# Performance work log

Measured on AMD Instinct MI355X. Metric: run time of the kernel, lower is better.

Reference implementation:

```python
import jax, jax.numpy as jnp
import numpy as np

B, H, S, DH = 2, 16, 2048, 64
MASK_FILL = -10000.0


def setup_inputs() -> dict:
    key = jax.random.key(0)
    kq, kk, kv = jax.random.split(key, 3)
    q = jax.random.normal(kq, (B, H, S, DH), dtype=jnp.float32)
    k = jax.random.normal(kk, (B, H, S, DH), dtype=jnp.float32)
    v = jax.random.normal(kv, (B, H, S, DH), dtype=jnp.float32)
    # causal mask: True where attention is disallowed (upper triangle)
    mask = jnp.triu(jnp.ones((S, S), dtype=jnp.bool_), k=1)
    return {"q": q, "k": k, "v": v, "mask": mask}


def reference(q, k, v, mask):
    scale = 1.0 / jnp.sqrt(jnp.asarray(k.shape[-1], dtype=q.dtype))
    # scores: [B, H, S_q, S_k]
    scores = jnp.einsum("bhqd,bhkd->bhqk", q, k) * scale
    # additive mask: masked_fill on a zeros [S_k, S_v] matrix -> -10000 where mask
    attn_bias = jnp.where(mask, jnp.asarray(MASK_FILL, dtype=k.dtype),
                          jnp.asarray(0.0, dtype=k.dtype))
    scores = scores + attn_bias  # broadcast over batch/heads
    attn = jax.nn.softmax(scores, axis=-1)
    # dropout_rate = 0.0 -> identity
    return jnp.einsum("bhqk,bhkd->bhqd", attn, v)
```

## Files before the change

### kernel.cpp

```cpp
#include <hip/hip_runtime.h>


#define S_LEN  2048
#define DHDIM  64
#define NHEADS 32
#define LDP    72
#define M2     23.083120654223414f
#define QSCALE 0.18033688011117658f
#define NSLOT  52

typedef __attribute__((ext_vector_type(8))) short bf16x8;
typedef __attribute__((ext_vector_type(4))) float f32x4;

#define RT(qt,k0,k1,sl) ((unsigned)(qt)<<24 | (unsigned)(k0)<<16 | (unsigned)(k1)<<8 | (unsigned)(sl))
__device__ __constant__ unsigned RTAB[63] = {
    RT(31,0,11,49),  RT(31,11,22,50), RT(30,0,11,46),  RT(21,0,11,20),
    RT(21,11,22,21), RT(20,0,11,18),  RT(10,0,11,255),
    RT(31,22,32,51), RT(30,11,21,47), RT(30,21,31,48), RT(29,0,10,43),
    RT(29,10,20,44), RT(29,20,30,45), RT(28,0,10,40),  RT(28,10,20,41),
    RT(27,0,10,37),  RT(20,11,21,19), RT(19,0,10,16),  RT(19,10,20,17),
    RT(18,0,10,14),  RT(9,0,10,255),
    RT(28,20,29,42), RT(27,10,19,38), RT(27,19,28,39), RT(26,0,9,34),
    RT(26,9,18,35),  RT(26,18,27,36), RT(25,0,9,31),   RT(25,9,18,32),
    RT(24,0,9,28),   RT(18,10,19,15), RT(17,0,9,12),   RT(17,9,18,13),
    RT(16,0,9,10),   RT(8,0,9,255),
    RT(25,18,26,33), RT(24,9,17,29),  RT(24,17,25,30), RT(23,0,8,25),
    RT(23,8,16,26),  RT(23,16,24,27), RT(22,0,8,22),   RT(22,8,16,23),
    RT(16,9,17,11),  RT(15,0,8,8),    RT(15,8,16,9),   RT(14,0,8,6),
    RT(7,0,8,255),
    RT(22,16,23,24), RT(14,8,15,7),   RT(13,0,7,4),    RT(13,7,14,5),
    RT(12,0,7,2),    RT(6,0,7,255),
    RT(12,7,13,3),   RT(11,0,6,0),    RT(11,6,12,1),   RT(5,0,6,255),
    RT(4,0,5,255),   RT(3,0,4,255),   RT(2,0,3,255),   RT(1,0,2,255),
    RT(0,0,1,255)};

__device__ __forceinline__ float fast_exp2(float x) {
#if __has_builtin(__builtin_amdgcn_exp2f)
    return __builtin_amdgcn_exp2f(x);
#else
    return exp2f(x);
#endif
}
__device__ __forceinline__ unsigned short f2bf(float f) {
    unsigned u = __float_as_uint(f);
    return (unsigned short)((u + 0x7fffu + ((u >> 16) & 1u)) >> 16);
}
__device__ __forceinline__ void ld8(const float* p, float* f) {
    float4 a = *(const float4*)p, b = *(const float4*)(p + 4);
    f[0]=a.x; f[1]=a.y; f[2]=a.z; f[3]=a.w; f[4]=b.x; f[5]=b.y; f[6]=b.z; f[7]=b.w;
}
__device__ __forceinline__ uint4 pack8(const float* f, float scale) {
    union { uint4 v; unsigned short s[8]; } w;
    #pragma unroll
    for (int j = 0; j < 8; j++) w.s[j] = f2bf(f[j] * scale);
    return w.v;
}
__device__ __forceinline__ unsigned packhi(float a, float b) {
#if __has_builtin(__builtin_amdgcn_perm)
    return __builtin_amdgcn_perm(__float_as_uint(b), __float_as_uint(a), 0x07060302u);
#else
    return (__float_as_uint(a) >> 16) | (__float_as_uint(b) & 0xffff0000u);
#endif
}

__global__ __launch_bounds__(256) void prep(
    const float* __restrict__ Qf, const float* __restrict__ Kf,
    const float* __restrict__ Vf, unsigned short* __restrict__ qb,
    unsigned short* __restrict__ kb, unsigned short* __restrict__ vtb)
{
    const int st = blockIdx.x, bh = blockIdx.y;
    __shared__ unsigned lt32[64][LDP / 2];
    const float* vp = Vf + ((size_t)bh * S_LEN + st * 64) * DHDIM;
    {
        const int c = threadIdx.x;
        const int sp = c >> 3;
        const int d0 = (c & 7) * 8;
        float fa[8], fb[8];
        ld8(vp + (2 * sp) * DHDIM + d0, fa);
        ld8(vp + (2 * sp + 1) * DHDIM + d0, fb);
        #pragma unroll
        for (int j = 0; j < 8; j++) {
            int d = d0 + j;
            int colw = (sp & 3) | ((((sp >> 2) ^ (d >> 3)) & 7) << 2);
            lt32[d][colw] = (unsigned)f2bf(fa[j]) | ((unsigned)f2bf(fb[j]) << 16);
        }
    }
    size_t off = ((size_t)(bh * 32 + st) * 4096) + (size_t)threadIdx.x * 16;
    float f[8];
    ld8(Qf + off, f);     *(uint4*)(qb + off)     = pack8(f, QSCALE);
    ld8(Qf + off + 8, f); *(uint4*)(qb + off + 8) = pack8(f, QSCALE);
    ld8(Kf + off, f);     *(uint4*)(kb + off)     = pack8(f, 1.0f);
    ld8(Kf + off + 8, f); *(uint4*)(kb + off + 8) = pack8(f, 1.0f);
    __syncthreads();
    unsigned short* op = vtb + (size_t)bh * DHDIM * S_LEN + st * 64;
    for (int c = threadIdx.x; c < 512; c += 256) {
        int d = c >> 3, q = c & 7;
        int colw = ((q ^ (d >> 3)) & 7) << 2;
        *(uint4*)(op + (size_t)d * S_LEN + q * 8) = *(const uint4*)&lt32[d][colw];
    }
}

__global__ __launch_bounds__(256) void fattn_splitk(
    const unsigned short* __restrict__ Qp, const unsigned short* __restrict__ Kp,
    const unsigned short* __restrict__ Vp,
    float* __restrict__ pO, float* __restrict__ pL, float* __restrict__ O)
{
    __shared__ unsigned short smem[192 * LDP];
    unsigned short (*ks)[LDP]  = (unsigned short(*)[LDP])smem;
    unsigned short (*vts)[LDP] = (unsigned short(*)[LDP])(smem + 64 * LDP);
    unsigned short (*qs)[LDP]  = (unsigned short(*)[LDP])(smem + 128 * LDP);
    unsigned short (*pst)[LDP] = qs;

    const int bh   = blockIdx.x;
    const unsigned e = RTAB[blockIdx.y];
    const int qt   = e >> 24;
    const int k0   = (e >> 16) & 255;
    const int k1   = (e >> 8) & 255;
    const int sl   = e & 255;
    const bool whole = (sl == 255);

    const int tid = threadIdx.x;
    const int wave = tid >> 6, lane = tid & 63;
    const int quad = lane >> 4, l16 = lane & 15;

    {
        const unsigned short* src = Qp + ((size_t)bh * S_LEN + qt * 64) * DHDIM;
        for (int c = tid; c < 512; c += 256) {
            int row = c >> 3, c8 = (c & 7) * 8;
            *(uint4*)&qs[row][c8] = *(const uint4*)(src + row * DHDIM + c8);
        }
    }
    __syncthreads();

    const int prow = wave * 16 + l16;
    const bf16x8 bq0 = *(const bf16x8*)&qs[prow][quad * 8];
    const bf16x8 bq1 = *(const bf16x8*)&qs[prow][32 + quad * 8];

    bf16x8 ones;
    #pragma unroll
    for (int j = 0; j < 8; j++) ones[j] = (short)0x3F80;

    f32x4 of[4];
    f32x4 of_l = (f32x4){0.f, 0.f, 0.f, 0.f};
    #pragma unroll
    for (int n = 0; n < 4; n++) of[n] = (f32x4){0.f, 0.f, 0.f, 0.f};

    const unsigned short* Kbh = Kp + (size_t)bh * S_LEN * DHDIM;
    const unsigned short* Vbh = Vp + (size_t)bh * DHDIM * S_LEN;
    const int sr = tid >> 3, sc = (tid & 7) * 8;
    uint4 kr0, kr1, vr0, vr1;
    {
        const unsigned short* ksrc = Kbh + (size_t)k0 * 64 * DHDIM;
        const unsigned short* vsrc = Vbh + k0 * 64;
        kr0 = *(const uint4*)(ksrc + sr * DHDIM + sc);
        kr1 = *(const uint4*)(ksrc + (sr + 32) * DHDIM + sc);
        vr0 = *(const uint4*)(vsrc + (size_t)sr * S_LEN + sc);
        vr1 = *(const uint4*)(vsrc + (size_t)(sr + 32) * S_LEN + sc);
    }

    for (int kt = k0; kt < k1; kt++) {
        __syncthreads();

        *(uint4*)&ks[sr][sc]       = kr0;
        *(uint4*)&ks[sr + 32][sc]  = kr1;
        *(uint4*)&vts[sr][sc]      = vr0;
        *(uint4*)&vts[sr + 32][sc] = vr1;

        if (kt + 1 < k1) {
            const unsigned short* ksrc = Kbh + (size_t)(kt + 1) * 64 * DHDIM;
            const unsigned short* vsrc = Vbh + (kt + 1) * 64;
            kr0 = *(const uint4*)(ksrc + sr * DHDIM + sc);
            kr1 = *(const uint4*)(ksrc + (sr + 32) * DHDIM + sc);
            vr0 = *(const uint4*)(vsrc + (size_t)sr * S_LEN + sc);
            vr1 = *(const uint4*)(vsrc + (size_t)(sr + 32) * S_LEN + sc);
        }
        __syncthreads();

        __builtin_amdgcn_s_setprio(1);
        f32x4 sf[4];
        #pragma unroll
        for (int n = 0; n < 4; n++) {
            bf16x8 ak0 = *(const bf16x8*)&ks[n * 16 + l16][quad * 8];
            bf16x8 ak1 = *(const bf16x8*)&ks[n * 16 + l16][32 + quad * 8];
            sf[n] = (f32x4){-M2, -M2, -M2, -M2};
            sf[n] = __builtin_amdgcn_mfma_f32_16x16x32_bf16(ak0, bq0, sf[n], 0, 0, 0);
            sf[n] = __builtin_amdgcn_mfma_f32_16x16x32_bf16(ak1, bq1, sf[n], 0, 0, 0);
        }
        __builtin_amdgcn_s_setprio(0);

        const bool diag = (kt == qt);
        #pragma unroll
        for (int n = 0; n < 4; n++) {
            float p[4];
            #pragma unroll
            for (int r = 0; r < 4; r++) {
                p[r] = fast_exp2(sf[n][r]);
                if (diag && (n * 16 + quad * 4 + r > prow)) p[r] = 0.f;
            }
            uint2 dw;
            dw.x = packhi(p[0], p[1]);
            dw.y = packhi(p[2], p[3]);
            *(uint2*)&pst[prow][n * 16 + quad * 4] = dw;
        }
        asm volatile("s_waitcnt lgkmcnt(0)" ::: "memory");

        __builtin_amdgcn_s_setprio(1);
        bf16x8 bp0 = *(const bf16x8*)&pst[prow][quad * 8];
        bf16x8 bp1 = *(const bf16x8*)&pst[prow][32 + quad * 8];
        of_l = __builtin_amdgcn_mfma_f32_16x16x32_bf16(ones, bp0, of_l, 0, 0, 0);
        of_l = __builtin_amdgcn_mfma_f32_16x16x32_bf16(ones, bp1, of_l, 0, 0, 0);
        #pragma unroll
        for (int n = 0; n < 4; n++) {
            bf16x8 av0 = *(const bf16x8*)&vts[n * 16 + l16][quad * 8];
            bf16x8 av1 = *(const bf16x8*)&vts[n * 16 + l16][32 + quad * 8];
            of[n] = __builtin_amdgcn_mfma_f32_16x16x32_bf16(av0, bp0, of[n], 0, 0, 0);
            of[n] = __builtin_amdgcn_mfma_f32_16x16x32_bf16(av1, bp1, of[n], 0, 0, 0);
        }
        __builtin_amdgcn_s_setprio(0);
    }

    if (whole) {
        const float inv = 1.f / of_l[0];
        float* op = O + ((size_t)bh * S_LEN + qt * 64 + prow) * DHDIM;
        #pragma unroll
        for (int n = 0; n < 4; n++)
            *(float4*)(op + n * 16 + quad * 4) = make_float4(
                of[n][0] * inv, of[n][1] * inv, of[n][2] * inv, of[n][3] * inv);
    } else {
        const int slot = bh * NSLOT + sl;
        if (quad == 0) pL[slot * 64 + prow] = of_l[0];
        float* op = pO + (size_t)slot * 4096 + prow * 64;
        #pragma unroll
        for (int n = 0; n < 4; n++)
            *(float4*)(op + n * 16 + quad * 4) =
                make_float4(of[n][0], of[n][1], of[n][2], of[n][3]);
    }
}

__global__ __launch_bounds__(256) void combine(
    const float* __restrict__ pO, const float* __restrict__ pL,
    float* __restrict__ O)
{
    const int qt = 11 + blockIdx.x, bh = blockIdx.y;
    int base, cnt;
    if (qt < 22) { base = (qt - 11) * 2;      cnt = 2; }
    else         { base = 22 + 3 * (qt - 22); cnt = 3; }
    const int sb = bh * NSLOT + base;
    const float* A = pO + (size_t)sb * 4096;
    float* out = O + ((size_t)bh * S_LEN + qt * 64) * DHDIM;
    #pragma unroll
    for (int k = 0; k < 4; k++) {
        int c = threadIdx.x + k * 256;
        int row = c >> 4;
        float l = pL[sb * 64 + row] + pL[(sb + 1) * 64 + row];
        float4 a = *(const float4*)(A + c * 4);
        float4 b = *(const float4*)(A + 4096 + c * 4);
        float4 s = make_float4(a.x + b.x, a.y + b.y, a.z + b.z, a.w + b.w);
        if (cnt == 3) {
            l += pL[(sb + 2) * 64 + row];
            float4 d = *(const float4*)(A + 8192 + c * 4);
            s = make_float4(s.x + d.x, s.y + d.y, s.z + d.z, s.w + d.w);
        }
        float inv = 1.f / l;
        *(float4*)(out + c * 4) = make_float4(
            s.x * inv, s.y * inv, s.z * inv, s.w * inv);
    }
}

template <bool PRE>
__global__ __launch_bounds__(256) void fattn_kernel(
    const void* __restrict__ Qp, const void* __restrict__ Kp,
    const void* __restrict__ Vp, float* __restrict__ O)
{
    __shared__ unsigned short smem[192 * LDP];
    unsigned short (*ks)[LDP]  = (unsigned short(*)[LDP])smem;
    unsigned short (*vts)[LDP] = (unsigned short(*)[LDP])(smem + 64 * LDP);
    unsigned short (*qs)[LDP]  = (unsigned short(*)[LDP])(smem + 128 * LDP);
    unsigned short (*pst)[LDP] = qs;

    const int id = blockIdx.y * 32 + blockIdx.x;
    const int g  = id >> 8;
    const int r8 = id & 255;
    const int bh = r8 >> 3;
    const int s8 = r8 & 7;
    const int qt = (g == 0) ? 31 - 2 * s8 : (g == 1) ? 2 * s8
                 : (g == 2) ? 30 - 2 * s8 : 2 * s8 + 1;

    const int tid = threadIdx.x;
    const int wave = tid >> 6, lane = tid & 63;
    const int quad = lane >> 4, l16 = lane & 15;

    if constexpr (PRE) {
        const unsigned short* src = (const unsigned short*)Qp
            + ((size_t)bh * S_LEN + qt * 64) * DHDIM;
        for (int c = tid; c < 512; c += 256) {
            int row = c >> 3, c8 = (c & 7) * 8;
            *(uint4*)&qs[row][c8] = *(const uint4*)(src + row * DHDIM + c8);
        }
    } else {
        const float* src = (const float*)Qp + ((size_t)bh * S_LEN + qt * 64) * DHDIM;
        for (int c = tid; c < 512; c += 256) {
            int row = c >> 3, c8 = (c & 7) * 8;
            float f[8]; ld8(src + row * DHDIM + c8, f);
            *(uint4*)&qs[row][c8] = pack8(f, QSCALE);
        }
    }
    __syncthreads();

    const int prow = wave * 16 + l16;
    const bf16x8 bq0 = *(const bf16x8*)&qs[prow][quad * 8];
    const bf16x8 bq1 = *(const bf16x8*)&qs[prow][32 + quad * 8];

    float l_p = 0.f;
    f32x4 of[4];
    #pragma unroll
    for (int n = 0; n < 4; n++) of[n] = (f32x4){0.f, 0.f, 0.f, 0.f};

    for (int kt = 0; kt <= qt; kt++) {
        __syncthreads();
        if constexpr (PRE) {
            const unsigned short* ksrc = (const unsigned short*)Kp
                + ((size_t)bh * S_LEN + kt * 64) * DHDIM;
            const unsigned short* vsrc = (const unsigned short*)Vp
                + (size_t)bh * DHDIM * S_LEN + kt * 64;
            for (int c = tid; c < 512; c += 256) {
                int row = c >> 3, c8 = (c & 7) * 8;
                *(uint4*)&ks[row][c8]  = *(const uint4*)(ksrc + row * DHDIM + c8);
                *(uint4*)&vts[row][c8] = *(const uint4*)(vsrc + (size_t)row * S_LEN + c8);
            }
        } else {
            const float* ksrc = (const float*)Kp + ((size_t)bh * S_LEN + kt * 64) * DHDIM;
            const float* vsrc = (const float*)Vp + ((size_t)bh * S_LEN + kt * 64) * DHDIM;
            for (int c = tid; c < 512; c += 256) {
                int row = c >> 3, c8 = (c & 7) * 8;
                float f[8];
                ld8(ksrc + row * DHDIM + c8, f);
                *(uint4*)&ks[row][c8] = pack8(f, 1.0f);
                ld8(vsrc + row * DHDIM + c8, f);
                #pragma unroll
                for (int j = 0; j < 8; j++) vts[c8 + j][row] = f2bf(f[j]);
            }
        }
        __syncthreads();

        f32x4 sf[4];
        #pragma unroll
        for (int n = 0; n < 4; n++) {
            bf16x8 ak0 = *(const bf16x8*)&ks[n * 16 + l16][quad * 8];
            bf16x8 ak1 = *(const bf16x8*)&ks[n * 16 + l16][32 + quad * 8];
            sf[n] = (f32x4){-M2, -M2, -M2, -M2};
            sf[n] = __builtin_amdgcn_mfma_f32_16x16x32_bf16(ak0, bq0, sf[n], 0, 0, 0);
            sf[n] = __builtin_amdgcn_mfma_f32_16x16x32_bf16(ak1, bq1, sf[n], 0, 0, 0);
        }

        const bool diag = (kt == qt);
        #pragma unroll
        for (int n = 0; n < 4; n++) {
            float p[4];
            #pragma unroll
            for (int r = 0; r < 4; r++) {
                p[r] = fast_exp2(sf[n][r]);
                if (diag && (n * 16 + quad * 4 + r > prow)) p[r] = 0.f;
                l_p += p[r];
            }
            uint2 dw;
            dw.x = packhi(p[0], p[1]);
            dw.y = packhi(p[2], p[3]);
            *(uint2*)&pst[prow][n * 16 + quad * 4] = dw;
        }
        asm volatile("s_waitcnt lgkmcnt(0)" ::: "memory");

        bf16x8 bp0 = *(const bf16x8*)&pst[prow][quad * 8];
        bf16x8 bp1 = *(const bf16x8*)&pst[prow][32 + quad * 8];
        #pragma unroll
        for (int n = 0; n < 4; n++) {
            bf16x8 av0 = *(const bf16x8*)&vts[n * 16 + l16][quad * 8];
            bf16x8 av1 = *(const bf16x8*)&vts[n * 16 + l16][32 + quad * 8];
            of[n] = __builtin_amdgcn_mfma_f32_16x16x32_bf16(av0, bp0, of[n], 0, 0, 0);
            of[n] = __builtin_amdgcn_mfma_f32_16x16x32_bf16(av1, bp1, of[n], 0, 0, 0);
        }
    }

    l_p += __shfl_xor(l_p, 16);
    l_p += __shfl_xor(l_p, 32);
    const float inv = 1.f / l_p;
    float* op = O + ((size_t)bh * S_LEN + qt * 64 + prow) * DHDIM;
    #pragma unroll
    for (int n = 0; n < 4; n++)
        *(float4*)(op + n * 16 + quad * 4) = make_float4(
            of[n][0] * inv, of[n][1] * inv, of[n][2] * inv, of[n][3] * inv);
}

extern "C" void kernel_launch(void* const* d_in, const int* in_sizes, int n_in,
                              void* d_out, int out_size, void* d_ws, size_t ws_size,
                              hipStream_t stream) {
    const float* Q = (const float*)d_in[0];
    const float* K = (const float*)d_in[1];
    const float* V = (const float*)d_in[2];
    float* O = (float*)d_out;
    const size_t N = (size_t)NHEADS * S_LEN * DHDIM;
    const size_t prepB  = 3 * N * sizeof(unsigned short);
    const size_t partB  = (size_t)NSLOT * 32 * (4096 + 64) * sizeof(float);

    if (d_ws && ws_size >= prepB + partB) {
        unsigned short* qb  = (unsigned short*)d_ws;
        unsigned short* kb  = qb + N;
        unsigned short* vtb = kb + N;
        float* pO = (float*)((char*)d_ws + prepB);
        float* pL = pO + (size_t)NSLOT * 32 * 4096;
        prep<<<dim3(S_LEN / 64, NHEADS), 256, 0, stream>>>(Q, K, V, qb, kb, vtb);
        fattn_splitk<<<dim3(32, 63), 256, 0, stream>>>(qb, kb, vtb, pO, pL, O);
        combine<<<dim3(21, 32), 256, 0, stream>>>(pO, pL, O);
    } else if (d_ws && ws_size >= prepB) {
        unsigned short* qb  = (unsigned short*)d_ws;
        unsigned short* kb  = qb + N;
        unsigned short* vtb = kb + N;
        prep<<<dim3(S_LEN / 64, NHEADS), 256, 0, stream>>>(Q, K, V, qb, kb, vtb);
        fattn_kernel<true><<<dim3(32, 32), 256, 0, stream>>>(qb, kb, vtb, O);
    } else {
        fattn_kernel<false><<<dim3(32, 32), 256, 0, stream>>>(Q, K, V, O);
    }
}
```

Measured before the change: 141.0 us.

## Process two K/V tiles per loop iteration with doubled shared buffers

The split-K attention loop now stages two 64-row K/V tiles per iteration into separate shared-memory buffers and prefetches the next two tiles into registers. This halves the number of barrier pairs per block and lets both QK^T MFMA batches issue back to back before the softmax/PV phases. In exchange, shared memory grows from 192 to 320 rows, and the extra prefetch registers and score accumulators raise register pressure, which may reduce occupancy.

Measured after the change: 144.7 us. 1.03x slower.

```diff
diff --git a/kernel.cpp b/kernel.cpp
--- a/kernel.cpp
+++ b/kernel.cpp
@@ -105,11 +105,13 @@
     const unsigned short* __restrict__ Vp,
     float* __restrict__ pO, float* __restrict__ pL, float* __restrict__ O)
 {
-    __shared__ unsigned short smem[192 * LDP];
-    unsigned short (*ks)[LDP]  = (unsigned short(*)[LDP])smem;
-    unsigned short (*vts)[LDP] = (unsigned short(*)[LDP])(smem + 64 * LDP);
-    unsigned short (*qs)[LDP]  = (unsigned short(*)[LDP])(smem + 128 * LDP);
-    unsigned short (*pst)[LDP] = qs;
+    __shared__ unsigned short smem[320 * LDP];
+    unsigned short (*ksA)[LDP]  = (unsigned short(*)[LDP])smem;
+    unsigned short (*ksB)[LDP]  = (unsigned short(*)[LDP])(smem + 64 * LDP);
+    unsigned short (*vtsA)[LDP] = (unsigned short(*)[LDP])(smem + 128 * LDP);
+    unsigned short (*vtsB)[LDP] = (unsigned short(*)[LDP])(smem + 192 * LDP);
+    unsigned short (*qs)[LDP]   = (unsigned short(*)[LDP])(smem + 256 * LDP);
+    unsigned short (*pst)[LDP]  = qs;
 
     const int bh   = blockIdx.x;
     const unsigned e = RTAB[blockIdx.y];
@@ -148,75 +150,142 @@
     const unsigned short* Kbh = Kp + (size_t)bh * S_LEN * DHDIM;
     const unsigned short* Vbh = Vp + (size_t)bh * DHDIM * S_LEN;
     const int sr = tid >> 3, sc = (tid & 7) * 8;
-    uint4 kr0, kr1, vr0, vr1;
+    uint4 krA0, krA1, vrA0, vrA1, krB0, krB1, vrB0, vrB1;
     {
         const unsigned short* ksrc = Kbh + (size_t)k0 * 64 * DHDIM;
         const unsigned short* vsrc = Vbh + k0 * 64;
-        kr0 = *(const uint4*)(ksrc + sr * DHDIM + sc);
-        kr1 = *(const uint4*)(ksrc + (sr + 32) * DHDIM + sc);
-        vr0 = *(const uint4*)(vsrc + (size_t)sr * S_LEN + sc);
-        vr1 = *(const uint4*)(vsrc + (size_t)(sr + 32) * S_LEN + sc);
-    }
-
-    for (int kt = k0; kt < k1; kt++) {
+        krA0 = *(const uint4*)(ksrc + sr * DHDIM + sc);
+        krA1 = *(const uint4*)(ksrc + (sr + 32) * DHDIM + sc);
+        vrA0 = *(const uint4*)(vsrc + (size_t)sr * S_LEN + sc);
+        vrA1 = *(const uint4*)(vsrc + (size_t)(sr + 32) * S_LEN + sc);
+    }
+    if (k0 + 1 < k1) {
+        const unsigned short* ksrc = Kbh + (size_t)(k0 + 1) * 64 * DHDIM;
+        const unsigned short* vsrc = Vbh + (k0 + 1) * 64;
+        krB0 = *(const uint4*)(ksrc + sr * DHDIM + sc);
+        krB1 = *(const uint4*)(ksrc + (sr + 32) * DHDIM + sc);
+        vrB0 = *(const uint4*)(vsrc + (size_t)sr * S_LEN + sc);
+        vrB1 = *(const uint4*)(vsrc + (size_t)(sr + 32) * S_LEN + sc);
+    }
+
+    for (int kt = k0; kt < k1; kt += 2) {
+        const bool hasB = (kt + 1 < k1);
         __syncthreads();
 
-        *(uint4*)&ks[sr][sc]       = kr0;
-        *(uint4*)&ks[sr + 32][sc]  = kr1;
-        *(uint4*)&vts[sr][sc]      = vr0;
-        *(uint4*)&vts[sr + 32][sc] = vr1;
-
-        if (kt + 1 < k1) {
-            const unsigned short* ksrc = Kbh + (size_t)(kt + 1) * 64 * DHDIM;
-            const unsigned short* vsrc = Vbh + (kt + 1) * 64;
-            kr0 = *(const uint4*)(ksrc + sr * DHDIM + sc);
-            kr1 = *(const uint4*)(ksrc + (sr + 32) * DHDIM + sc);
-            vr0 = *(const uint4*)(vsrc + (size_t)sr * S_LEN + sc);
-            vr1 = *(const uint4*)(vsrc + (size_t)(sr + 32) * S_LEN + sc);
+        *(uint4*)&ksA[sr][sc]       = krA0;
+        *(uint4*)&ksA[sr + 32][sc]  = krA1;
+        *(uint4*)&vtsA[sr][sc]      = vrA0;
+        *(uint4*)&vtsA[sr + 32][sc] = vrA1;
+        if (hasB) {
+            *(uint4*)&ksB[sr][sc]       = krB0;
+            *(uint4*)&ksB[sr + 32][sc]  = krB1;
+            *(uint4*)&vtsB[sr][sc]      = vrB0;
+            *(uint4*)&vtsB[sr + 32][sc] = vrB1;
+        }
+
+        if (kt + 2 < k1) {
+            const unsigned short* ksrc = Kbh + (size_t)(kt + 2) * 64 * DHDIM;
+            const unsigned short* vsrc = Vbh + (kt + 2) * 64;
+            krA0 = *(const uint4*)(ksrc + sr * DHDIM + sc);
+            krA1 = *(const uint4*)(ksrc + (sr + 32) * DHDIM + sc);
+            vrA0 = *(const uint4*)(vsrc + (size_t)sr * S_LEN + sc);
+            vrA1 = *(const uint4*)(vsrc + (size_t)(sr + 32) * S_LEN + sc);
+        }
+        if (kt + 3 < k1) {
+            const unsigned short* ksrc = Kbh + (size_t)(kt + 3) * 64 * DHDIM;
+            const unsigned short* vsrc = Vbh + (kt + 3) * 64;
+            krB0 = *(const uint4*)(ksrc + sr * DHDIM + sc);
+            krB1 = *(const uint4*)(ksrc + (sr + 32) * DHDIM + sc);
+            vrB0 = *(const uint4*)(vsrc + (size_t)sr * S_LEN + sc);
+            vrB1 = *(const uint4*)(vsrc + (size_t)(sr + 32) * S_LEN + sc);
         }
         __syncthreads();
 
         __builtin_amdgcn_s_setprio(1);
-        f32x4 sf[4];
+        f32x4 sfA[4], sfB[4];
         #pragma unroll
         for (int n = 0; n < 4; n++) {
-            bf16x8 ak0 = *(const bf16x8*)&ks[n * 16 + l16][quad * 8];
-            bf16x8 ak1 = *(const bf16x8*)&ks[n * 16 + l16][32 + quad * 8];
-            sf[n] = (f32x4){-M2, -M2, -M2, -M2};
-            sf[n] = __builtin_amdgcn_mfma_f32_16x16x32_bf16(ak0, bq0, sf[n], 0, 0, 0);
-            sf[n] = __builtin_amdgcn_mfma_f32_16x16x32_bf16(ak1, bq1, sf[n], 0, 0, 0);
+            bf16x8 ak0 = *(const bf16x8*)&ksA[n * 16 + l16][quad * 8];
+            bf16x8 ak1 = *(const bf16x8*)&ksA[n * 16 + l16][32 + quad * 8];
+            sfA[n] = (f32x4){-M2, -M2, -M2, -M2};
+            sfA[n] = __builtin_amdgcn_mfma_f32_16x16x32_bf16(ak0, bq0, sfA[n], 0, 0, 0);
+            sfA[n] = __builtin_amdgcn_mfma_f32_16x16x32_bf16(ak1, bq1, sfA[n], 0, 0, 0);
+        }
+        if (hasB) {
+            #pragma unroll
+            for (int n = 0; n < 4; n++) {
+                bf16x8 bk0 = *(const bf16x8*)&ksB[n * 16 + l16][quad * 8];
+                bf16x8 bk1 = *(const bf16x8*)&ksB[n * 16 + l16][32 + quad * 8];
+                sfB[n] = (f32x4){-M2, -M2, -M2, -M2};
+                sfB[n] = __builtin_amdgcn_mfma_f32_16x16x32_bf16(bk0, bq0, sfB[n], 0, 0, 0);
+                sfB[n] = __builtin_amdgcn_mfma_f32_16x16x32_bf16(bk1, bq1, sfB[n], 0, 0, 0);
+            }
         }
         __builtin_amdgcn_s_setprio(0);
 
-        const bool diag = (kt == qt);
-        #pragma unroll
-        for (int n = 0; n < 4; n++) {
-            float p[4];
-            #pragma unroll
-            for (int r = 0; r < 4; r++) {
-                p[r] = fast_exp2(sf[n][r]);
-                if (diag && (n * 16 + quad * 4 + r > prow)) p[r] = 0.f;
-            }
-            uint2 dw;
-            dw.x = packhi(p[0], p[1]);
-            dw.y = packhi(p[2], p[3]);
-            *(uint2*)&pst[prow][n * 16 + quad * 4] = dw;
-        }
-        asm volatile("s_waitcnt lgkmcnt(0)" ::: "memory");
-
-        __builtin_amdgcn_s_setprio(1);
-        bf16x8 bp0 = *(const bf16x8*)&pst[prow][quad * 8];
-        bf16x8 bp1 = *(const bf16x8*)&pst[prow][32 + quad * 8];
-        of_l = __builtin_amdgcn_mfma_f32_16x16x32_bf16(ones, bp0, of_l, 0, 0, 0);
-        of_l = __builtin_amdgcn_mfma_f32_16x16x32_bf16(ones, bp1, of_l, 0, 0, 0);
-        #pragma unroll
-        for (int n = 0; n < 4; n++) {
-            bf16x8 av0 = *(const bf16x8*)&vts[n * 16 + l16][quad * 8];
-            bf16x8 av1 = *(const bf16x8*)&vts[n * 16 + l16][32 + quad * 8];
-            of[n] = __builtin_amdgcn_mfma_f32_16x16x32_bf16(av0, bp0, of[n], 0, 0, 0);
-            of[n] = __builtin_amdgcn_mfma_f32_16x16x32_bf16(av1, bp1, of[n], 0, 0, 0);
-        }
-        __builtin_amdgcn_s_setprio(0);
+        {
+            const bool diag = (kt == qt);
+            #pragma unroll
+            for (int n = 0; n < 4; n++) {
+                float p[4];
+                #pragma unroll
+                for (int r = 0; r < 4; r++) {
+                    p[r] = fast_exp2(sfA[n][r]);
+                    if (diag && (n * 16 + quad * 4 + r > prow)) p[r] = 0.f;
+                }
+                uint2 dw;
+                dw.x = packhi(p[0], p[1]);
+                dw.y = packhi(p[2], p[3]);
+                *(uint2*)&pst[prow][n * 16 + quad * 4] = dw;
+            }
+            asm volatile("s_waitcnt lgkmcnt(0)" ::: "memory");
+
+            __builtin_amdgcn_s_setprio(1);
+            bf16x8 bp0 = *(const bf16x8*)&pst[prow][quad * 8];
+            bf16x8 bp1 = *(const bf16x8*)&pst[prow][32 + quad * 8];
+            of_l = __builtin_amdgcn_mfma_f32_16x16x32_bf16(ones, bp0, of_l, 0, 0, 0);
+            of_l = __builtin_amdgcn_mfma_f32_16x16x32_bf16(ones, bp1, of_l, 0, 0, 0);
+            #pragma unroll
+            for (int n = 0; n < 4; n++) {
+                bf16x8 av0 = *(const bf16x8*)&vtsA[n * 16 + l16][quad * 8];
+                bf16x8 av1 = *(const bf16x8*)&vtsA[n * 16 + l16][32 + quad * 8];
+                of[n] = __builtin_amdgcn_mfma_f32_16x16x32_bf16(av0, bp0, of[n], 0, 0, 0);
+                of[n] = __builtin_amdgcn_mfma_f32_16x16x32_bf16(av1, bp1, of[n], 0, 0, 0);
+            }
+            __builtin_amdgcn_s_setprio(0);
+        }
+
+        if (hasB) {
+            const bool diag = (kt + 1 == qt);
+            #pragma unroll
+            for (int n = 0; n < 4; n++) {
+                float p[4];
+                #pragma unroll
+                for (int r = 0; r < 4; r++) {
+                    p[r] = fast_exp2(sfB[n][r]);
+                    if (diag && (n * 16 + quad * 4 + r > prow)) p[r] = 0.f;
+                }
+                uint2 dw;
+                dw.x = packhi(p[0], p[1]);
+                dw.y = packhi(p[2], p[3]);
+                *(uint2*)&pst[prow][n * 16 + quad * 4] = dw;
+            }
+            asm volatile("s_waitcnt lgkmcnt(0)" ::: "memory");
+
+            __builtin_amdgcn_s_setprio(1);
+            bf16x8 bp0 = *(const bf16x8*)&pst[prow][quad * 8];
+            bf16x8 bp1 = *(const bf16x8*)&pst[prow][32 + quad * 8];
+            of_l = __builtin_amdgcn_mfma_f32_16x16x32_bf16(ones, bp0, of_l, 0, 0, 0);
+            of_l = __builtin_amdgcn_mfma_f32_16x16x32_bf16(ones, bp1, of_l, 0, 0, 0);
+            #pragma unroll
+            for (int n = 0; n < 4; n++) {
+                bf16x8 av0 = *(const bf16x8*)&vtsB[n * 16 + l16][quad * 8];
+                bf16x8 av1 = *(const bf16x8*)&vtsB[n * 16 + l16][32 + quad * 8];
+                of[n] = __builtin_amdgcn_mfma_f32_16x16x32_bf16(av0, bp0, of[n], 0, 0, 0);
+                of[n] = __builtin_amdgcn_mfma_f32_16x16x32_bf16(av1, bp1, of[n], 0, 0, 0);
+            }
+            __builtin_amdgcn_s_setprio(0);
+        }
     }
 
     if (whole) {
```

## Switch attention kernel to 32x32 MFMA tiles with software-pipelined PV stage

Applied to the files above, without the earlier changes.

Replaces the 16x16x32 MFMA tiling with 32x32x16 MFMAs. Each wave now covers a 32-query by 32-key quadrant, and Q fragments are loaded straight from global memory into registers instead of staging through LDS. The P·V product for the previous key tile is deferred one iteration, with double-buffered V and P LDS regions, so it overlaps with the next QK^T and exp stage and the explicit lgkmcnt wait goes away. The cost is more LDS per block, a launch-bounds occupancy hint, and an extra epilogue step to drain the last tile.

Measured after the change: 141.7 us. Within noise of the previous version (+0.5%).

```diff
diff --git a/kernel.cpp b/kernel.cpp
--- a/kernel.cpp
+++ b/kernel.cpp
@@ -11,6 +11,7 @@
 
 typedef __attribute__((ext_vector_type(8))) short bf16x8;
 typedef __attribute__((ext_vector_type(4))) float f32x4;
+typedef __attribute__((ext_vector_type(16))) float f32x16;
 
 #define RT(qt,k0,k1,sl) ((unsigned)(qt)<<24 | (unsigned)(k0)<<16 | (unsigned)(k1)<<8 | (unsigned)(sl))
 __device__ __constant__ unsigned RTAB[63] = {
@@ -100,16 +101,17 @@
     }
 }
 
-__global__ __launch_bounds__(256) void fattn_splitk(
+__global__ __launch_bounds__(256, 3) void fattn_splitk(
     const unsigned short* __restrict__ Qp, const unsigned short* __restrict__ Kp,
     const unsigned short* __restrict__ Vp,
     float* __restrict__ pO, float* __restrict__ pL, float* __restrict__ O)
 {
-    __shared__ unsigned short smem[192 * LDP];
-    unsigned short (*ks)[LDP]  = (unsigned short(*)[LDP])smem;
-    unsigned short (*vts)[LDP] = (unsigned short(*)[LDP])(smem + 64 * LDP);
-    unsigned short (*qs)[LDP]  = (unsigned short(*)[LDP])(smem + 128 * LDP);
-    unsigned short (*pst)[LDP] = qs;
+    __shared__ unsigned short smem[320 * LDP];
+    unsigned short (*ks)[LDP]   = (unsigned short(*)[LDP])smem;
+    unsigned short (*vtsA)[LDP] = (unsigned short(*)[LDP])(smem + 64 * LDP);
+    unsigned short (*vtsB)[LDP] = (unsigned short(*)[LDP])(smem + 128 * LDP);
+    unsigned short (*pstA)[LDP] = (unsigned short(*)[LDP])(smem + 192 * LDP);
+    unsigned short (*pstB)[LDP] = (unsigned short(*)[LDP])(smem + 256 * LDP);
 
     const int bh   = blockIdx.x;
     const unsigned e = RTAB[blockIdx.y];
@@ -119,31 +121,26 @@
     const int sl   = e & 255;
     const bool whole = (sl == 255);
 
-    const int tid = threadIdx.x;
+    const int tid  = threadIdx.x;
     const int wave = tid >> 6, lane = tid & 63;
-    const int quad = lane >> 4, l16 = lane & 15;
-
-    {
-        const unsigned short* src = Qp + ((size_t)bh * S_LEN + qt * 64) * DHDIM;
-        for (int c = tid; c < 512; c += 256) {
-            int row = c >> 3, c8 = (c & 7) * 8;
-            *(uint4*)&qs[row][c8] = *(const uint4*)(src + row * DHDIM + c8);
-        }
-    }
-    __syncthreads();
-
-    const int prow = wave * 16 + l16;
-    const bf16x8 bq0 = *(const bf16x8*)&qs[prow][quad * 8];
-    const bf16x8 bq1 = *(const bf16x8*)&qs[prow][32 + quad * 8];
+    const int q31  = lane & 31, hi = lane >> 5;
+    const int qh   = wave & 1, kh = wave >> 1;
+    const int qrow = qh * 32 + q31;
+
+    const unsigned short* qsrc = Qp + ((size_t)bh * S_LEN + qt * 64 + qrow) * DHDIM;
+    const bf16x8 bq0 = *(const bf16x8*)(qsrc + hi * 8);
+    const bf16x8 bq1 = *(const bf16x8*)(qsrc + 16 + hi * 8);
+    const bf16x8 bq2 = *(const bf16x8*)(qsrc + 32 + hi * 8);
+    const bf16x8 bq3 = *(const bf16x8*)(qsrc + 48 + hi * 8);
 
     bf16x8 ones;
     #pragma unroll
     for (int j = 0; j < 8; j++) ones[j] = (short)0x3F80;
 
-    f32x4 of[4];
-    f32x4 of_l = (f32x4){0.f, 0.f, 0.f, 0.f};
-    #pragma unroll
-    for (int n = 0; n < 4; n++) of[n] = (f32x4){0.f, 0.f, 0.f, 0.f};
+    f32x16 of, ofl;
+    #pragma unroll
+    for (int i = 0; i < 16; i++) { of[i] = 0.f; ofl[i] = 0.f; }
+    unsigned pdw[8];
 
     const unsigned short* Kbh = Kp + (size_t)bh * S_LEN * DHDIM;
     const unsigned short* Vbh = Vp + (size_t)bh * DHDIM * S_LEN;
@@ -161,11 +158,21 @@
     for (int kt = k0; kt < k1; kt++) {
         __syncthreads();
 
-        *(uint4*)&ks[sr][sc]       = kr0;
-        *(uint4*)&ks[sr + 32][sc]  = kr1;
-        *(uint4*)&vts[sr][sc]      = vr0;
-        *(uint4*)&vts[sr + 32][sc] = vr1;
-
+        *(uint4*)&ks[sr][sc]      = kr0;
+        *(uint4*)&ks[sr + 32][sc] = kr1;
+        {
+            unsigned short (*vts)[LDP] = (kt & 1) ? vtsB : vtsA;
+            *(uint4*)&vts[sr][sc]      = vr0;
+            *(uint4*)&vts[sr + 32][sc] = vr1;
+        }
+        if (kt > k0) {
+            unsigned short (*pst)[LDP] = ((kt - 1) & 1) ? pstB : pstA;
+            const int cb = kh * 32 + 4 * hi;
+            *(uint2*)&pst[qrow][cb +  0] = *(uint2*)&pdw[0];
+            *(uint2*)&pst[qrow][cb +  8] = *(uint2*)&pdw[2];
+            *(uint2*)&pst[qrow][cb + 16] = *(uint2*)&pdw[4];
+            *(uint2*)&pst[qrow][cb + 24] = *(uint2*)&pdw[6];
+        }
         if (kt + 1 < k1) {
             const unsigned short* ksrc = Kbh + (size_t)(kt + 1) * 64 * DHDIM;
             const unsigned short* vsrc = Vbh + (kt + 1) * 64;
@@ -176,64 +183,93 @@
         }
         __syncthreads();
 
+        if (kt > k0) {
+            const unsigned short (*pst)[LDP] = ((kt - 1) & 1) ? pstB : pstA;
+            const unsigned short (*vts)[LDP] = ((kt - 1) & 1) ? vtsB : vtsA;
+            __builtin_amdgcn_s_setprio(1);
+            #pragma unroll
+            for (int s = 0; s < 4; s++) {
+                bf16x8 av = *(const bf16x8*)&vts[kh * 32 + q31][s * 16 + hi * 8];
+                bf16x8 bp = *(const bf16x8*)&pst[qrow][s * 16 + hi * 8];
+                of  = __builtin_amdgcn_mfma_f32_32x32x16_bf16(av, bp, of, 0, 0, 0);
+                ofl = __builtin_amdgcn_mfma_f32_32x32x16_bf16(ones, bp, ofl, 0, 0, 0);
+            }
+            __builtin_amdgcn_s_setprio(0);
+        }
+
+        f32x16 sf;
+        #pragma unroll
+        for (int i = 0; i < 16; i++) sf[i] = -M2;
         __builtin_amdgcn_s_setprio(1);
-        f32x4 sf[4];
-        #pragma unroll
-        for (int n = 0; n < 4; n++) {
-            bf16x8 ak0 = *(const bf16x8*)&ks[n * 16 + l16][quad * 8];
-            bf16x8 ak1 = *(const bf16x8*)&ks[n * 16 + l16][32 + quad * 8];
-            sf[n] = (f32x4){-M2, -M2, -M2, -M2};
-            sf[n] = __builtin_amdgcn_mfma_f32_16x16x32_bf16(ak0, bq0, sf[n], 0, 0, 0);
-            sf[n] = __builtin_amdgcn_mfma_f32_16x16x32_bf16(ak1, bq1, sf[n], 0, 0, 0);
+        {
+            bf16x8 ak = *(const bf16x8*)&ks[kh * 32 + q31][hi * 8];
+            sf = __builtin_amdgcn_mfma_f32_32x32x16_bf16(ak, bq0, sf, 0, 0, 0);
+            ak = *(const bf16x8*)&ks[kh * 32 + q31][16 + hi * 8];
+            sf = __builtin_amdgcn_mfma_f32_32x32x16_bf16(ak, bq1, sf, 0, 0, 0);
+            ak = *(const bf16x8*)&ks[kh * 32 + q31][32 + hi * 8];
+            sf = __builtin_amdgcn_mfma_f32_32x32x16_bf16(ak, bq2, sf, 0, 0, 0);
+            ak = *(const bf16x8*)&ks[kh * 32 + q31][48 + hi * 8];
+            sf = __builtin_amdgcn_mfma_f32_32x32x16_bf16(ak, bq3, sf, 0, 0, 0);
         }
         __builtin_amdgcn_s_setprio(0);
 
         const bool diag = (kt == qt);
         #pragma unroll
-        for (int n = 0; n < 4; n++) {
+        for (int g = 0; g < 4; g++) {
             float p[4];
             #pragma unroll
-            for (int r = 0; r < 4; r++) {
-                p[r] = fast_exp2(sf[n][r]);
-                if (diag && (n * 16 + quad * 4 + r > prow)) p[r] = 0.f;
+            for (int r2 = 0; r2 < 4; r2++) {
+                float pv = fast_exp2(sf[g * 4 + r2]);
+                if (diag) {
+                    const int kl = kh * 32 + 8 * g + 4 * hi + r2;
+                    if (kl > qrow) pv = 0.f;
+                }
+                p[r2] = pv;
             }
-            uint2 dw;
-            dw.x = packhi(p[0], p[1]);
-            dw.y = packhi(p[2], p[3]);
-            *(uint2*)&pst[prow][n * 16 + quad * 4] = dw;
-        }
-        asm volatile("s_waitcnt lgkmcnt(0)" ::: "memory");
-
+            pdw[g * 2]     = packhi(p[0], p[1]);
+            pdw[g * 2 + 1] = packhi(p[2], p[3]);
+        }
+    }
+
+    {
+        unsigned short (*pst)[LDP] = ((k1 - 1) & 1) ? pstB : pstA;
+        const int cb = kh * 32 + 4 * hi;
+        *(uint2*)&pst[qrow][cb +  0] = *(uint2*)&pdw[0];
+        *(uint2*)&pst[qrow][cb +  8] = *(uint2*)&pdw[2];
+        *(uint2*)&pst[qrow][cb + 16] = *(uint2*)&pdw[4];
+        *(uint2*)&pst[qrow][cb + 24] = *(uint2*)&pdw[6];
+        __syncthreads();
+        const unsigned short (*pstc)[LDP] = ((k1 - 1) & 1) ? pstB : pstA;
+        const unsigned short (*vts)[LDP]  = ((k1 - 1) & 1) ? vtsB : vtsA;
         __builtin_amdgcn_s_setprio(1);
-        bf16x8 bp0 = *(const bf16x8*)&pst[prow][quad * 8];
-        bf16x8 bp1 = *(const bf16x8*)&pst[prow][32 + quad * 8];
-        of_l = __builtin_amdgcn_mfma_f32_16x16x32_bf16(ones, bp0, of_l, 0, 0, 0);
-        of_l = __builtin_amdgcn_mfma_f32_16x16x32_bf16(ones, bp1, of_l, 0, 0, 0);
-        #pragma unroll
-        for (int n = 0; n < 4; n++) {
-            bf16x8 av0 = *(const bf16x8*)&vts[n * 16 + l16][quad * 8];
-            bf16x8 av1 = *(const bf16x8*)&vts[n * 16 + l16][32 + quad * 8];
-            of[n] = __builtin_amdgcn_mfma_f32_16x16x32_bf16(av0, bp0, of[n], 0, 0, 0);
-            of[n] = __builtin_amdgcn_mfma_f32_16x16x32_bf16(av1, bp1, of[n], 0, 0, 0);
+        #pragma unroll
+        for (int s = 0; s < 4; s++) {
+            bf16x8 av = *(const bf16x8*)&vts[kh * 32 + q31][s * 16 + hi * 8];
+            bf16x8 bp = *(const bf16x8*)&pstc[qrow][s * 16 + hi * 8];
+            of  = __builtin_amdgcn_mfma_f32_32x32x16_bf16(av, bp, of, 0, 0, 0);
+            ofl = __builtin_amdgcn_mfma_f32_32x32x16_bf16(ones, bp, ofl, 0, 0, 0);
         }
         __builtin_amdgcn_s_setprio(0);
     }
 
+    const float l = ofl[0];
     if (whole) {
-        const float inv = 1.f / of_l[0];
-        float* op = O + ((size_t)bh * S_LEN + qt * 64 + prow) * DHDIM;
-        #pragma unroll
-        for (int n = 0; n < 4; n++)
-            *(float4*)(op + n * 16 + quad * 4) = make_float4(
-                of[n][0] * inv, of[n][1] * inv, of[n][2] * inv, of[n][3] * inv);
+        const float inv = 1.f / l;
+        float* op = O + ((size_t)bh * S_LEN + qt * 64 + qrow) * DHDIM
+                  + kh * 32 + 4 * hi;
+        #pragma unroll
+        for (int g = 0; g < 4; g++)
+            *(float4*)(op + 8 * g) = make_float4(
+                of[4 * g] * inv, of[4 * g + 1] * inv,
+                of[4 * g + 2] * inv, of[4 * g + 3] * inv);
     } else {
         const int slot = bh * NSLOT + sl;
-        if (quad == 0) pL[slot * 64 + prow] = of_l[0];
-        float* op = pO + (size_t)slot * 4096 + prow * 64;
-        #pragma unroll
-        for (int n = 0; n < 4; n++)
-            *(float4*)(op + n * 16 + quad * 4) =
-                make_float4(of[n][0], of[n][1], of[n][2], of[n][3]);
+        if (kh == 0 && hi == 0) pL[slot * 64 + qrow] = l;
+        float* op = pO + (size_t)slot * 4096 + qrow * 64 + kh * 32 + 4 * hi;
+        #pragma unroll
+        for (int g = 0; g < 4; g++)
+            *(float4*)(op + 8 * g) = make_float4(
+                of[4 * g], of[4 * g + 1], of[4 * g + 2], of[4 * g + 3]);
     }
 }
 
```
